# Kernel tuning notes

Hardware: AMD Instinct MI355X
Metric: run time of the kernel (lower is better)

## Reference

```python
import jax, jax.numpy as jnp
import numpy as np

HEADS, BS, HALO = 8, 8, 3
WIN = BS + 2 * HALO  # 14


def setup_inputs() -> dict:
    key = jax.random.key(0)
    k1, k2, k3, k4 = jax.random.split(key, 4)
    B, C, H, W = 16, 256, 64, 64
    dim_out_qk, dim_out_v = 256, 256
    std = C ** (-0.5)
    x = jax.random.normal(k1, (B, C, H, W), jnp.float32)
    Wq = jax.random.normal(k2, (dim_out_qk, C), jnp.float32) * std
    Wkv = jax.random.normal(k3, (dim_out_qk + dim_out_v, C), jnp.float32) * std
    pos_bias = jax.random.normal(k4, (HEADS, BS * BS, WIN * WIN), jnp.float32) * 0.02
    return {"x": x, "Wq": Wq, "Wkv": Wkv, "pos_bias": pos_bias}


def reference(x, Wq, Wkv, pos_bias):
    B, C, H, W = x.shape
    dhqk = Wq.shape[0] // HEADS            # 32
    dhv = Wkv.shape[0] // HEADS - dhqk     # 32
    scale = dhqk ** (-0.5)
    nhb, nwb = H // BS, W // BS
    nb = nhb * nwb

    xl = jnp.transpose(x, (0, 2, 3, 1))    # [B, H, W, C]

    # queries: [B, heads, nb, bs^2, dhqk] (row-major within block)
    q = xl @ Wq.T
    q = q.reshape(B, nhb, BS, nwb, BS, HEADS, dhqk)
    q = q.transpose(0, 5, 1, 3, 2, 4, 6).reshape(B, HEADS, nb, BS * BS, dhqk)

    # keys/values via overlapping halo windows (zero-padded unfold)
    kv = xl @ Wkv.T                                       # [B, H, W, dim_kv]
    kv = jnp.pad(kv, ((0, 0), (HALO, HALO), (HALO, HALO), (0, 0)))
    ridx = (jnp.arange(nhb) * BS)[:, None] + jnp.arange(WIN)[None, :]
    cidx = (jnp.arange(nwb) * BS)[:, None] + jnp.arange(WIN)[None, :]
    kv = kv[:, ridx]
    kv = kv[:, :, :, cidx]
    kv = kv.transpose(0, 1, 3, 2, 4, 5).reshape(B, nb, WIN * WIN, HEADS, dhqk + dhv)
    k = kv[..., :dhqk]
    v = kv[..., dhqk:]

    attn = jnp.einsum('bhnqd,bnkhd->bhnqk', q, k) * scale + pos_bias[None, :, None]
    attn = jax.nn.softmax(attn, axis=-1)
    out = jnp.einsum('bhnqk,bnkhd->bhnqd', attn, v)       # [B, heads, nb, bs^2, dhv]

    out = out.reshape(B, HEADS, nhb, nwb, BS, BS, dhv)
    out = out.transpose(0, 1, 6, 2, 4, 3, 5).reshape(B, HEADS * dhv, H, W)
    return out
```

## Files before the change

### kernel.cpp

```cpp
#include <hip/hip_runtime.h>
#include <hip/hip_bf16.h>
#include <stdint.h>

#define HEADS 8
#define WIN 14
#define NPOS 196
#define NPAD 224
#define NB 16
#define NC 256
#define NH 64
#define NW 64
#define NP 4096
#define NKV 512
#define NOC 768

typedef __bf16 bf16_t;
typedef bf16_t bf16x8 __attribute__((ext_vector_type(8)));
typedef float f32x4 __attribute__((ext_vector_type(4)));

union Frag {
  uint4 u4;
  bf16x8 b8;
  ushort us[8];
};

__device__ __forceinline__ ushort f2bf(float f) {
  bf16_t h = (bf16_t)f;
  return __builtin_bit_cast(ushort, h);
}
__device__ __forceinline__ bf16x8 load_bf8(const float* __restrict__ p) {
  float4 a = *reinterpret_cast<const float4*>(p);
  float4 b = *reinterpret_cast<const float4*>(p + 4);
  bf16x8 r;
  r[0] = (bf16_t)a.x; r[1] = (bf16_t)a.y; r[2] = (bf16_t)a.z; r[3] = (bf16_t)a.w;
  r[4] = (bf16_t)b.x; r[5] = (bf16_t)b.y; r[6] = (bf16_t)b.z; r[7] = (bf16_t)b.w;
  return r;
}

__device__ __forceinline__ void gload_lds16(const ushort* g, ushort* l) {
#if __has_builtin(__builtin_amdgcn_global_load_lds)
  __builtin_amdgcn_global_load_lds(
      (const __attribute__((address_space(1))) unsigned int*)(const void*)g,
      (__attribute__((address_space(3))) unsigned int*)(void*)l, 16, 0, 0);
#else
  *reinterpret_cast<uint4*>(l) = *reinterpret_cast<const uint4*>(g);
#endif
}

__device__ ushort g_wb[NOC * NC];
__device__ float g_pbt[HEADS * 64 * NPAD];

__global__ __launch_bounds__(256) void k_prep(const float* __restrict__ wq,
                                              const float* __restrict__ wkv,
                                              const float* __restrict__ pb) {
  const int wg = blockIdx.x;
  if (wg < 96) {
    int idx = (wg * 256 + threadIdx.x) * 8;
    int oc = idx >> 8, c = idx & 255;
    const float* src = (oc < 256) ? (wq + (size_t)oc * NC + c)
                                  : (wkv + (size_t)(oc - 256) * NC + c);
    Frag v;
    v.b8 = load_bf8(src);
    *reinterpret_cast<uint4*>(g_wb + idx) = v.u4;
  } else {
    int row = wg - 96;
    int key = threadIdx.x;
    if (key < NPAD) {
      float v = -100000.0f;
      if (key < NPOS) v = pb[(size_t)row * NPOS + key] * 1.4426950408889634f;
      g_pbt[(size_t)row * NPAD + key] = v;
    }
  }
}

__global__ __launch_bounds__(256) void k_xt(const float* __restrict__ x,
                                            ushort* __restrict__ xt) {
  __shared__ __align__(16) ushort ls[64][66];
  const int b = blockIdx.z, p0 = blockIdx.x * 64, c0 = blockIdx.y * 64;
  const int by8 = blockIdx.y * 8;
  const int tid = threadIdx.x;
  #pragma unroll
  for (int it = 0; it < 4; ++it) {
    int i = it * 256 + tid;
    int c = i >> 4, ps = (i & 15) * 4;
    float4 v = *reinterpret_cast<const float4*>(x + ((size_t)(b * NC + c0 + c)) * NP + p0 + ps);
    ls[ps + 0][c] = f2bf(v.x);
    ls[ps + 1][c] = f2bf(v.y);
    ls[ps + 2][c] = f2bf(v.z);
    ls[ps + 3][c] = f2bf(v.w);
  }
  __syncthreads();
  #pragma unroll
  for (int it = 0; it < 2; ++it) {
    int i = it * 256 + tid;
    int p = i >> 3, gl = i & 7;
    Frag o;
    #pragma unroll
    for (int j = 0; j < 8; ++j) o.us[j] = ls[p][gl * 8 + j];
    int gph = by8 + (gl ^ (p & 7));
    *reinterpret_cast<uint4*>(xt + ((size_t)(b * NP) + p0 + p) * NC + gph * 8) = o.u4;
  }
}

__global__ __launch_bounds__(256, 2) void k_proj2(const ushort* __restrict__ xt,
                                                  ushort* __restrict__ qkv) {
  __shared__ __align__(16) ushort As[128 * 256];
  const int row0 = blockIdx.x * 128;
  const int n0 = blockIdx.y * 256;
  const int tid = threadIdx.x, lane = tid & 63, wid = tid >> 6;
  const int quad = lane >> 4, lc = lane & 15;
  const ushort* gs = xt + (size_t)row0 * NC;
  #pragma unroll
  for (int it = 0; it < 16; ++it) {
    int f = it * 256 + tid;
    gload_lds16(gs + (size_t)f * 8, As + f * 8);
  }
  __syncthreads();
  const int wm = (wid & 1) * 64, wn = (wid >> 1) * 128;
  f32x4 acc[4][8] = {};
  #pragma unroll
  for (int ks = 0; ks < 8; ++ks) {
    const int k0 = ks * 32 + quad * 8;
    Frag a[4];
    #pragma unroll
    for (int mt = 0; mt < 4; ++mt) {
      int row = wm + mt * 16 + lc;
      int gk = (ks * 4 + quad) ^ (lc & 7);
      a[mt].u4 = *reinterpret_cast<const uint4*>(&As[row * 256 + gk * 8]);
    }
    #pragma unroll
    for (int ng = 0; ng < 2; ++ng) {
      Frag bb[4];
      #pragma unroll
      for (int j = 0; j < 4; ++j) {
        int oc = n0 + wn + (ng * 4 + j) * 16 + lc;
        bb[j].u4 = *reinterpret_cast<const uint4*>(g_wb + (size_t)oc * NC + k0);
      }
      #pragma unroll
      for (int mt = 0; mt < 4; ++mt)
        #pragma unroll
        for (int j = 0; j < 4; ++j)
          acc[mt][ng * 4 + j] = __builtin_amdgcn_mfma_f32_16x16x32_bf16(
              a[mt].b8, bb[j].b8, acc[mt][ng * 4 + j], 0, 0, 0);
    }
  }
  __syncthreads();
  #pragma unroll
  for (int mt = 0; mt < 4; ++mt)
    #pragma unroll
    for (int nn = 0; nn < 8; ++nn) {
      int row = wm + mt * 16 + quad * 4;
      #pragma unroll
      for (int r = 0; r < 4; ++r) {
        int rr = row + r;
        int col = wn + nn * 16 + lc;
        As[rr * 256 + (((col >> 3) ^ (rr & 7)) * 8) + (col & 7)] = f2bf(acc[mt][nn][r]);
      }
    }
  __syncthreads();
  #pragma unroll
  for (int it = 0; it < 16; ++it) {
    int i = it * 256 + tid;
    int r = i >> 5, g = i & 31;
    uint4 u = *reinterpret_cast<const uint4*>(&As[r * 256 + ((g ^ (r & 7)) * 8)]);
    *reinterpret_cast<uint4*>(qkv + ((size_t)(row0 + r)) * NOC + n0 + g * 8) = u;
  }
}

__global__ __launch_bounds__(256) void k_attn_f2(const ushort* __restrict__ qkv,
                                                 float* __restrict__ out) {
  __shared__ __align__(16) ushort ksh[NPAD][40];
  __shared__ __align__(16) ushort vth[32][232];
  __shared__ __align__(16) ushort psh[4][16][32];
  float (*osh)[33] = reinterpret_cast<float(*)[33]>(&ksh[0][0]);
  const int orig = blockIdx.x;
  const int wgid = (orig & 7) * 1024 + (orig >> 3);
  const int h = wgid & 7;
  const int blk = (wgid >> 3) & 63;
  const int b = wgid >> 9;
  const int by = blk >> 3, bx = blk & 7;
  const int tid = threadIdx.x, lane = tid & 63, w = tid >> 6;
  const int quad = lane >> 4, lc = lane & 15;

  Frag aq;
  {
    int q = w * 16 + lc;
    int py = by * 8 + (q >> 3), px = bx * 8 + (q & 7);
    aq.u4 = *reinterpret_cast<const uint4*>(
        qkv + ((size_t)(b * NP + py * NW + px)) * NOC + h * 32 + quad * 8);
  }

  #pragma unroll
  for (int it = 0; it < 7; ++it) {
    int i = it * 256 + tid;
    int pos = i >> 3, seg = i & 7;
    Frag v;
    v.u4 = make_uint4(0u, 0u, 0u, 0u);
    if (pos < NPOS) {
      int wy = pos / WIN;
      int wx = pos - wy * WIN;
      int yq = by * 8 - 3 + wy, xx = bx * 8 - 3 + wx;
      if ((unsigned)yq < (unsigned)NH && (unsigned)xx < (unsigned)NW)
        v.u4 = *reinterpret_cast<const uint4*>(
            qkv + ((size_t)(b * NP + yq * NW + xx)) * NOC + 256 + h * 64 + seg * 8);
    }
    if (seg < 4) {
      *reinterpret_cast<uint4*>(&ksh[pos][seg * 8]) = v.u4;
    } else {
      int d0 = (seg - 4) * 8;
      int cp = pos ^ ((seg - 4) << 3);
      #pragma unroll
      for (int j = 0; j < 8; ++j) vth[d0 + j][cp] = v.us[j];
    }
  }
  __syncthreads();

  f32x4 s[14];
  __builtin_amdgcn_s_setprio(1);
  #pragma unroll
  for (int nt = 0; nt < 14; ++nt) {
    Frag bk;
    bk.u4 = *reinterpret_cast<const uint4*>(&ksh[nt * 16 + lc][quad * 8]);
    f32x4 z = {0.f, 0.f, 0.f, 0.f};
    s[nt] = __builtin_amdgcn_mfma_f32_16x16x32_bf16(aq.b8, bk.b8, z, 0, 0, 0);
  }
  __builtin_amdgcn_s_setprio(0);

  const float ck = 0.17677669529663687f * 1.4426950408889634f;
  const int qi = w * 16 + quad * 4;
  const float* __restrict__ pbh = g_pbt + (size_t)(h * 64) * NPAD;
  float lsum[4] = {0.f, 0.f, 0.f, 0.f};
  #pragma unroll
  for (int nt = 0; nt < 14; ++nt) {
    int col = nt * 16 + lc;
    #pragma unroll
    for (int r = 0; r < 4; ++r) {
      float p = exp2f(s[nt][r] * ck + pbh[(size_t)(qi + r) * NPAD + col]);
      s[nt][r] = p;
      lsum[r] += p;
    }
  }

  f32x4 o[2] = {};
  #pragma unroll
  for (int kt = 0; kt < 7; ++kt) {
    #pragma unroll
    for (int t = 0; t < 2; ++t)
      #pragma unroll
      for (int r = 0; r < 4; ++r)
        psh[w][quad * 4 + r][t * 16 + lc] = f2bf(s[2 * kt + t][r]);
    Frag ap;
    ap.u4 = *reinterpret_cast<const uint4*>(&psh[w][lc][quad * 8]);
    __builtin_amdgcn_s_setprio(1);
    #pragma unroll
    for (int t = 0; t < 2; ++t) {
      int d = t * 16 + lc;
      int g = (kt * 4 + quad) ^ ((d >> 3) & 3);
      Frag bv;
      bv.u4 = *reinterpret_cast<const uint4*>(&vth[d][g * 8]);
      o[t] = __builtin_amdgcn_mfma_f32_16x16x32_bf16(ap.b8, bv.b8, o[t], 0, 0, 0);
    }
    __builtin_amdgcn_s_setprio(0);
  }

  #pragma unroll
  for (int m = 1; m < 16; m <<= 1)
    #pragma unroll
    for (int r = 0; r < 4; ++r) lsum[r] += __shfl_xor(lsum[r], m);
  float rinv[4];
  #pragma unroll
  for (int r = 0; r < 4; ++r) rinv[r] = 1.0f / lsum[r];

  __syncthreads();
  #pragma unroll
  for (int t = 0; t < 2; ++t)
    #pragma unroll
    for (int r = 0; r < 4; ++r)
      osh[w * 16 + quad * 4 + r][t * 16 + lc] = o[t][r] * rinv[r];
  __syncthreads();

  {
    int d = tid >> 3, yy = tid & 7;
    float4 o0, o1;
    o0.x = osh[yy * 8 + 0][d]; o0.y = osh[yy * 8 + 1][d];
    o0.z = osh[yy * 8 + 2][d]; o0.w = osh[yy * 8 + 3][d];
    o1.x = osh[yy * 8 + 4][d]; o1.y = osh[yy * 8 + 5][d];
    o1.z = osh[yy * 8 + 6][d]; o1.w = osh[yy * 8 + 7][d];
    float* op = out + ((size_t)(b * NC + h * 32 + d) * NH + by * 8 + yy) * NW + bx * 8;
    *reinterpret_cast<float4*>(op) = o0;
    *reinterpret_cast<float4*>(op + 4) = o1;
  }
}

__global__ __launch_bounds__(256) void k_proj_r4(const float* __restrict__ x,
                                                 const float* __restrict__ wq,
                                                 const float* __restrict__ wkv,
                                                 ushort* __restrict__ qkv) {
  __shared__ __align__(16) ushort As[64][264];
  const int b = blockIdx.z, y = blockIdx.x;
  const int n0 = blockIdx.y * 256;
  const int tid = threadIdx.x, lane = tid & 63, wid = tid >> 6;
  const int quad = lane >> 4, lc = lane & 15;
  #pragma unroll
  for (int it = 0; it < 16; ++it) {
    int i = it * 256 + tid;
    int c = i >> 4, xs = (i & 15) * 4;
    float4 v = *reinterpret_cast<const float4*>(x + ((size_t)(b * NC + c)) * NP + y * NW + xs);
    #pragma unroll
    for (int j = 0; j < 4; ++j) {
      int row = xs + j;
      float f = (j == 0) ? v.x : (j == 1) ? v.y : (j == 2) ? v.z : v.w;
      As[row][c ^ ((((row >> 2) & 3)) << 3)] = f2bf(f);
    }
  }
  __syncthreads();
  const int wm = (wid & 1) * 32, wn = (wid >> 1) * 128;
  const int swz = ((lc >> 2) & 3) << 3;
  f32x4 acc[2][8] = {};
  #pragma unroll
  for (int ks = 0; ks < 8; ++ks) {
    const int k0 = ks * 32 + quad * 8;
    Frag a0, a1;
    a0.u4 = *reinterpret_cast<const uint4*>(&As[wm + lc][k0 ^ swz]);
    a1.u4 = *reinterpret_cast<const uint4*>(&As[wm + 16 + lc][k0 ^ swz]);
    #pragma unroll
    for (int nh = 0; nh < 2; ++nh) {
      bf16x8 bb[4];
      #pragma unroll
      for (int nt = 0; nt < 4; ++nt) {
        int oc = n0 + wn + nh * 64 + nt * 16 + lc;
        const float* wp = (oc < 256) ? (wq + (size_t)oc * NC) : (wkv + (size_t)(oc - 256) * NC);
        bb[nt] = load_bf8(wp + k0);
      }
      #pragma unroll
      for (int nt = 0; nt < 4; ++nt) {
        acc[0][nh * 4 + nt] = __builtin_amdgcn_mfma_f32_16x16x32_bf16(a0.b8, bb[nt], acc[0][nh * 4 + nt], 0, 0, 0);
        acc[1][nh * 4 + nt] = __builtin_amdgcn_mfma_f32_16x16x32_bf16(a1.b8, bb[nt], acc[1][nh * 4 + nt], 0, 0, 0);
      }
    }
  }
  __syncthreads();
  #pragma unroll
  for (int mt = 0; mt < 2; ++mt)
    #pragma unroll
    for (int nn = 0; nn < 8; ++nn)
      #pragma unroll
      for (int r = 0; r < 4; ++r)
        As[wm + mt * 16 + quad * 4 + r][wn + nn * 16 + lc] = f2bf(acc[mt][nn][r]);
  __syncthreads();
  #pragma unroll
  for (int v8 = 0; v8 < 8; ++v8) {
    int flat = v8 * 256 + tid;
    int p = flat >> 5, seg = flat & 31;
    uint4 u = *reinterpret_cast<const uint4*>(&As[p][seg * 8]);
    *reinterpret_cast<uint4*>(qkv + ((size_t)(b * NP) + y * NW + p) * NOC + n0 + seg * 8) = u;
  }
}

__global__ __launch_bounds__(256) void k_kv(const float* __restrict__ x,
                                            const float* __restrict__ wkv,
                                            ushort* __restrict__ kvb) {
  __shared__ __align__(16) ushort As[64][264];
  const int b = blockIdx.z;
  const int y = blockIdx.x;
  const int n0 = blockIdx.y * 128;
  const int tid = threadIdx.x;
  const int lane = tid & 63, wid = tid >> 6;
  const int quad = lane >> 4, lc = lane & 15;
  #pragma unroll
  for (int it = 0; it < 16; ++it) {
    int i = it * 256 + tid;
    int c = i >> 4, xs = (i & 15) * 4;
    float4 v = *reinterpret_cast<const float4*>(x + ((size_t)(b * NC + c)) * NP + y * NW + xs);
    As[xs + 0][c] = f2bf(v.x);
    As[xs + 1][c] = f2bf(v.y);
    As[xs + 2][c] = f2bf(v.z);
    As[xs + 3][c] = f2bf(v.w);
  }
  __syncthreads();
  const int wm = (wid & 1) * 32, wn = (wid >> 1) * 64;
  f32x4 acc[2][4] = {};
  #pragma unroll
  for (int ks = 0; ks < 8; ++ks) {
    const int k0 = ks * 32 + quad * 8;
    Frag a[2];
    bf16x8 bb[4];
    #pragma unroll
    for (int mt = 0; mt < 2; ++mt)
      a[mt].u4 = *reinterpret_cast<const uint4*>(&As[wm + mt * 16 + lc][k0]);
    #pragma unroll
    for (int nt = 0; nt < 4; ++nt) {
      int oc = n0 + wn + nt * 16 + lc;
      bb[nt] = load_bf8(wkv + (size_t)oc * NC + k0);
    }
    #pragma unroll
    for (int mt = 0; mt < 2; ++mt)
      #pragma unroll
      for (int nt = 0; nt < 4; ++nt)
        acc[mt][nt] = __builtin_amdgcn_mfma_f32_16x16x32_bf16(a[mt].b8, bb[nt], acc[mt][nt], 0, 0, 0);
  }
  #pragma unroll
  for (int mt = 0; mt < 2; ++mt) {
    #pragma unroll
    for (int r = 0; r < 4; ++r) {
      int pl = wm + mt * 16 + quad * 4 + r;
      #pragma unroll
      for (int nt = 0; nt < 4; ++nt) {
        int oc = n0 + wn + nt * 16 + lc;
        kvb[((size_t)(b * NP + y * NW + pl)) * NKV + oc] = f2bf(acc[mt][nt][r]);
      }
    }
  }
}

__global__ __launch_bounds__(256) void k_attn_v3(const float* __restrict__ x,
                                                 const float* __restrict__ wq,
                                                 const ushort* __restrict__ kvb,
                                                 const float* __restrict__ pbias,
                                                 float* __restrict__ out) {
  __shared__ __align__(16) ushort ksh[NPAD][40];
  __shared__ __align__(16) ushort vth[32][232];
  __shared__ __align__(16) ushort psh[4][16][232];
  __shared__ __align__(16) ushort qsh[4][16][32];
  __shared__ __align__(16) float osh[64][33];
  const int b = blockIdx.z, h = blockIdx.y, blk = blockIdx.x;
  const int by = blk >> 3, bx = blk & 7;
  const int tid = threadIdx.x, lane = tid & 63, w = tid >> 6;
  const int quad = lane >> 4, lc = lane & 15;

  for (int it = 0; it < 7; ++it) {
    int i = it * 256 + tid;
    int pos = i >> 3, seg = i & 7;
    Frag v;
    v.u4 = make_uint4(0u, 0u, 0u, 0u);
    if (pos < NPOS) {
      int wy = pos / WIN;
      int wx = pos - wy * WIN;
      int yq = by * 8 - 3 + wy, xx = bx * 8 - 3 + wx;
      if ((unsigned)yq < (unsigned)NH && (unsigned)xx < (unsigned)NW)
        v.u4 = *reinterpret_cast<const uint4*>(
            kvb + ((size_t)(b * NP + yq * NW + xx)) * NKV + h * 64 + seg * 8);
    }
    if (seg < 4) {
      *reinterpret_cast<uint4*>(&ksh[pos][seg * 8]) = v.u4;
    } else {
      int d0 = (seg - 4) * 8;
      #pragma unroll
      for (int j = 0; j < 8; ++j) vth[d0 + j][pos] = v.us[j];
    }
  }

  f32x4 qacc[2] = {};
  {
    const int q = w * 16 + lc;
    const size_t p = (size_t)(by * 8 + (q >> 3)) * NW + bx * 8 + (q & 7);
    #pragma unroll
    for (int ks = 0; ks < 8; ++ks) {
      const int k0 = ks * 32 + quad * 8;
      Frag ax;
      #pragma unroll
      for (int j = 0; j < 8; ++j)
        ax.us[j] = f2bf(x[((size_t)(b * NC + k0 + j)) * NP + p]);
      bf16x8 bw0 = load_bf8(wq + (size_t)(h * 32 + lc) * NC + k0);
      bf16x8 bw1 = load_bf8(wq + (size_t)(h * 32 + 16 + lc) * NC + k0);
      qacc[0] = __builtin_amdgcn_mfma_f32_16x16x32_bf16(ax.b8, bw0, qacc[0], 0, 0, 0);
      qacc[1] = __builtin_amdgcn_mfma_f32_16x16x32_bf16(ax.b8, bw1, qacc[1], 0, 0, 0);
    }
  }
  #pragma unroll
  for (int t = 0; t < 2; ++t)
    #pragma unroll
    for (int r = 0; r < 4; ++r)
      qsh[w][quad * 4 + r][t * 16 + lc] = f2bf(qacc[t][r]);
  Frag aq;
  aq.u4 = *reinterpret_cast<const uint4*>(&qsh[w][lc][quad * 8]);

  __syncthreads();

  f32x4 s[14];
  #pragma unroll
  for (int nt = 0; nt < 14; ++nt) {
    Frag bk;
    bk.u4 = *reinterpret_cast<const uint4*>(&ksh[nt * 16 + lc][quad * 8]);
    f32x4 z = {0.f, 0.f, 0.f, 0.f};
    s[nt] = __builtin_amdgcn_mfma_f32_16x16x32_bf16(aq.b8, bk.b8, z, 0, 0, 0);
  }

  const float scale = 0.17677669529663687f;
  const int qi = w * 16 + quad * 4;
  float lsum[4] = {0.f, 0.f, 0.f, 0.f};
  #pragma unroll
  for (int nt = 0; nt < 14; ++nt) {
    int col = nt * 16 + lc;
    #pragma unroll
    for (int r = 0; r < 4; ++r) {
      float p = 0.f;
      if (col < NPOS)
        p = __expf(s[nt][r] * scale + pbias[(size_t)(h * 64 + qi + r) * NPOS + col]);
      s[nt][r] = p;
      lsum[r] += p;
    }
  }
  #pragma unroll
  for (int m = 1; m < 16; m <<= 1) {
    #pragma unroll
    for (int r = 0; r < 4; ++r) lsum[r] += __shfl_xor(lsum[r], m);
  }
  #pragma unroll
  for (int nt = 0; nt < 14; ++nt) {
    #pragma unroll
    for (int r = 0; r < 4; ++r) psh[w][quad * 4 + r][nt * 16 + lc] = f2bf(s[nt][r]);
  }
  f32x4 o[2] = {};
  #pragma unroll
  for (int kt = 0; kt < 7; ++kt) {
    Frag ap;
    ap.u4 = *reinterpret_cast<const uint4*>(&psh[w][lc][kt * 32 + quad * 8]);
    #pragma unroll
    for (int t = 0; t < 2; ++t) {
      Frag bv;
      bv.u4 = *reinterpret_cast<const uint4*>(&vth[t * 16 + lc][kt * 32 + quad * 8]);
      o[t] = __builtin_amdgcn_mfma_f32_16x16x32_bf16(ap.b8, bv.b8, o[t], 0, 0, 0);
    }
  }
  #pragma unroll
  for (int t = 0; t < 2; ++t)
    #pragma unroll
    for (int r = 0; r < 4; ++r)
      osh[w * 16 + quad * 4 + r][t * 16 + lc] = o[t][r] / lsum[r];
  __syncthreads();
  {
    int d = tid >> 3, yy = tid & 7;
    float4 o0, o1;
    o0.x = osh[yy * 8 + 0][d]; o0.y = osh[yy * 8 + 1][d];
    o0.z = osh[yy * 8 + 2][d]; o0.w = osh[yy * 8 + 3][d];
    o1.x = osh[yy * 8 + 4][d]; o1.y = osh[yy * 8 + 5][d];
    o1.z = osh[yy * 8 + 6][d]; o1.w = osh[yy * 8 + 7][d];
    float* op = out + ((size_t)(b * NC + h * 32 + d) * NH + by * 8 + yy) * NW + bx * 8;
    *reinterpret_cast<float4*>(op) = o0;
    *reinterpret_cast<float4*>(op + 4) = o1;
  }
}

extern "C" void kernel_launch(void* const* d_in, const int* in_sizes, int n_in,
                              void* d_out, int out_size, void* d_ws, size_t ws_size,
                              hipStream_t stream) {
  const float* x   = (const float*)d_in[0];
  const float* wq  = (const float*)d_in[1];
  const float* wkv = (const float*)d_in[2];
  const float* pb  = (const float*)d_in[3];
  float* outp = (float*)d_out;

  const size_t qkv_bytes = (size_t)NB * NP * NOC * sizeof(ushort);
  const size_t xt_bytes  = (size_t)NB * NP * NC * sizeof(ushort);

  if (ws_size >= qkv_bytes + xt_bytes) {
    ushort* qkv = (ushort*)d_ws;
    ushort* xt  = (ushort*)((char*)d_ws + qkv_bytes);
    k_prep<<<dim3(608), 256, 0, stream>>>(wq, wkv, pb);
    k_xt<<<dim3(NP / 64, NC / 64, NB), 256, 0, stream>>>(x, xt);
    k_proj2<<<dim3(NB * NP / 128, 3), 256, 0, stream>>>(xt, qkv);
    k_attn_f2<<<dim3(NB * HEADS * 64), 256, 0, stream>>>(qkv, outp);
  } else if (ws_size >= qkv_bytes) {
    ushort* qkv = (ushort*)d_ws;
    k_prep<<<dim3(608), 256, 0, stream>>>(wq, wkv, pb);
    k_proj_r4<<<dim3(NH, 3, NB), 256, 0, stream>>>(x, wq, wkv, qkv);
    k_attn_f2<<<dim3(NB * HEADS * 64), 256, 0, stream>>>(qkv, outp);
  } else {
    ushort* kvb = (ushort*)d_ws;
    k_kv<<<dim3(NH, NKV / 128, NB), 256, 0, stream>>>(x, wkv, kvb);
    k_attn_v3<<<dim3(64, HEADS, NB), 256, 0, stream>>>(x, wq, kvb, pb, outp);
  }
}
```

Measured before the change: 297.7 us.

## Transpose QK MFMA to keep P in registers and pre-swizzle position bias

The QK^T MFMA operands are swapped so each lane holds scores for four consecutive keys of one query. That lets the P fragment for the PV MFMA be built directly in registers, removing the LDS round-trip through psh. The position bias is re-laid out in the prep kernel to match the MFMA output layout, so each lane reads one float4 per tile instead of four strided scalars. The V reads become two 8-byte LDS loads with a matching swizzle, and the row-sum reduction is reworked to use fewer shuffles. The risk is that any mismatch between the new fragment layouts and the bias layout would give wrong results, and the split V loads add LDS instructions.

```diff
diff --git a/kernel.cpp b/kernel.cpp
--- a/kernel.cpp
+++ b/kernel.cpp
@@ -48,14 +48,15 @@
 }
 
 __device__ ushort g_wb[NOC * NC];
-__device__ float g_pbt[HEADS * 64 * NPAD];
+__device__ float g_pb2[HEADS * 4 * 14 * 256];
 
 __global__ __launch_bounds__(256) void k_prep(const float* __restrict__ wq,
                                               const float* __restrict__ wkv,
                                               const float* __restrict__ pb) {
   const int wg = blockIdx.x;
+  const int tid = threadIdx.x;
   if (wg < 96) {
-    int idx = (wg * 256 + threadIdx.x) * 8;
+    int idx = (wg * 256 + tid) * 8;
     int oc = idx >> 8, c = idx & 255;
     const float* src = (oc < 256) ? (wq + (size_t)oc * NC + c)
                                   : (wkv + (size_t)(oc - 256) * NC + c);
@@ -63,13 +64,19 @@
     v.b8 = load_bf8(src);
     *reinterpret_cast<uint4*>(g_wb + idx) = v.u4;
   } else {
-    int row = wg - 96;
-    int key = threadIdx.x;
-    if (key < NPAD) {
-      float v = -100000.0f;
-      if (key < NPOS) v = pb[(size_t)row * NPOS + key] * 1.4426950408889634f;
-      g_pbt[(size_t)row * NPAD + key] = v;
-    }
+    int idx2 = wg - 96;
+    int h = idx2 / 56;
+    int rem = idx2 - h * 56;
+    int w = rem / 14;
+    int nt = rem - w * 14;
+    int lane = tid >> 2, r = tid & 3;
+    int quad = lane >> 4, lc = lane & 15;
+    int q = w * 16 + lc;
+    int key = nt * 16 + quad * 4 + r;
+    float v = -100000.0f;
+    if (key < NPOS)
+      v = pb[((size_t)(h * 64 + q)) * NPOS + key] * 1.4426950408889634f;
+    g_pb2[(size_t)idx2 * 256 + tid] = v;
   }
 }
 
@@ -171,7 +178,6 @@
                                                  float* __restrict__ out) {
   __shared__ __align__(16) ushort ksh[NPAD][40];
   __shared__ __align__(16) ushort vth[32][232];
-  __shared__ __align__(16) ushort psh[4][16][32];
   float (*osh)[33] = reinterpret_cast<float(*)[33]>(&ksh[0][0]);
   const int orig = blockIdx.x;
   const int wgid = (orig & 7) * 1024 + (orig >> 3);
@@ -222,54 +228,51 @@
     Frag bk;
     bk.u4 = *reinterpret_cast<const uint4*>(&ksh[nt * 16 + lc][quad * 8]);
     f32x4 z = {0.f, 0.f, 0.f, 0.f};
-    s[nt] = __builtin_amdgcn_mfma_f32_16x16x32_bf16(aq.b8, bk.b8, z, 0, 0, 0);
+    s[nt] = __builtin_amdgcn_mfma_f32_16x16x32_bf16(bk.b8, aq.b8, z, 0, 0, 0);
   }
   __builtin_amdgcn_s_setprio(0);
 
   const float ck = 0.17677669529663687f * 1.4426950408889634f;
-  const int qi = w * 16 + quad * 4;
-  const float* __restrict__ pbh = g_pbt + (size_t)(h * 64) * NPAD;
-  float lsum[4] = {0.f, 0.f, 0.f, 0.f};
+  const float* __restrict__ pbw = g_pb2 + (size_t)((h * 4 + w) * 14) * 256;
+  float lsum = 0.f;
   #pragma unroll
   for (int nt = 0; nt < 14; ++nt) {
-    int col = nt * 16 + lc;
+    float4 bv4 = *reinterpret_cast<const float4*>(pbw + nt * 256 + lane * 4);
     #pragma unroll
     for (int r = 0; r < 4; ++r) {
-      float p = exp2f(s[nt][r] * ck + pbh[(size_t)(qi + r) * NPAD + col]);
+      float p = exp2f(s[nt][r] * ck + (&bv4.x)[r]);
       s[nt][r] = p;
-      lsum[r] += p;
+      lsum += p;
     }
   }
 
   f32x4 o[2] = {};
   #pragma unroll
   for (int kt = 0; kt < 7; ++kt) {
-    #pragma unroll
-    for (int t = 0; t < 2; ++t)
-      #pragma unroll
-      for (int r = 0; r < 4; ++r)
-        psh[w][quad * 4 + r][t * 16 + lc] = f2bf(s[2 * kt + t][r]);
-    Frag ap;
-    ap.u4 = *reinterpret_cast<const uint4*>(&psh[w][lc][quad * 8]);
-    __builtin_amdgcn_s_setprio(1);
+    Frag pa;
+    #pragma unroll
+    for (int j = 0; j < 8; ++j)
+      pa.us[j] = f2bf(s[2 * kt + (j >> 2)][j & 3]);
     #pragma unroll
     for (int t = 0; t < 2; ++t) {
       int d = t * 16 + lc;
-      int g = (kt * 4 + quad) ^ ((d >> 3) & 3);
+      int xr = ((d >> 3) & 3) << 3;
+      int c0 = (kt * 32 + quad * 4) ^ xr;
+      int c1 = (kt * 32 + 16 + quad * 4) ^ xr;
       Frag bv;
-      bv.u4 = *reinterpret_cast<const uint4*>(&vth[d][g * 8]);
-      o[t] = __builtin_amdgcn_mfma_f32_16x16x32_bf16(ap.b8, bv.b8, o[t], 0, 0, 0);
-    }
-    __builtin_amdgcn_s_setprio(0);
-  }
-
-  #pragma unroll
-  for (int m = 1; m < 16; m <<= 1)
-    #pragma unroll
-    for (int r = 0; r < 4; ++r) lsum[r] += __shfl_xor(lsum[r], m);
+      *reinterpret_cast<uint2*>(&bv.us[0]) = *reinterpret_cast<const uint2*>(&vth[d][c0]);
+      *reinterpret_cast<uint2*>(&bv.us[4]) = *reinterpret_cast<const uint2*>(&vth[d][c1]);
+      o[t] = __builtin_amdgcn_mfma_f32_16x16x32_bf16(pa.b8, bv.b8, o[t], 0, 0, 0);
+    }
+  }
+
+  lsum += __shfl_xor(lsum, 16);
+  lsum += __shfl_xor(lsum, 32);
+  float rl = 1.0f / lsum;
   float rinv[4];
   #pragma unroll
-  for (int r = 0; r < 4; ++r) rinv[r] = 1.0f / lsum[r];
+  for (int r = 0; r < 4; ++r)
+    rinv[r] = __shfl(rl, (lane & 48) + quad * 4 + r);
 
   __syncthreads();
   #pragma unroll
@@ -557,13 +560,13 @@
   if (ws_size >= qkv_bytes + xt_bytes) {
     ushort* qkv = (ushort*)d_ws;
     ushort* xt  = (ushort*)((char*)d_ws + qkv_bytes);
-    k_prep<<<dim3(608), 256, 0, stream>>>(wq, wkv, pb);
+    k_prep<<<dim3(544), 256, 0, stream>>>(wq, wkv, pb);
     k_xt<<<dim3(NP / 64, NC / 64, NB), 256, 0, stream>>>(x, xt);
     k_proj2<<<dim3(NB * NP / 128, 3), 256, 0, stream>>>(xt, qkv);
     k_attn_f2<<<dim3(NB * HEADS * 64), 256, 0, stream>>>(qkv, outp);
   } else if (ws_size >= qkv_bytes) {
     ushort* qkv = (ushort*)d_ws;
-    k_prep<<<dim3(608), 256, 0, stream>>>(wq, wkv, pb);
+    k_prep<<<dim3(544), 256, 0, stream>>>(wq, wkv, pb);
     k_proj_r4<<<dim3(NH, 3, NB), 256, 0, stream>>>(x, wq, wkv, qkv);
     k_attn_f2<<<dim3(NB * HEADS * 64), 256, 0, stream>>>(qkv, outp);
   } else {
```

Measured after the change: 289.0 us. 3.0% less time.
